# Kernel optimization log

Measured on AMD Instinct MI355X. Metric: run time of the kernel, lower is better.

The kernel has to match this reference:

```python
import jax, jax.numpy as jnp
import numpy as np
from jax import lax

B, ENC, H, E, V = 16, 64, 96, 128, 32000

def _same_pad(k):
    # PyTorch padding='same' (stride=1): low = (k-1)//2, high = (k-1) - low
    t = k - 1
    return (t // 2, t - t // 2)

def _conv(x, w, pad):
    return lax.conv_general_dilated(x, w, (1, 1), pad,
                                    dimension_numbers=('NCHW', 'OIHW', 'NCHW'))

def setup_inputs() -> dict:
    key = jax.random.key(0)
    ks = jax.random.split(key, 16)
    s = 0.05
    return {
        'encoder_outputs': jax.random.normal(ks[0], (B, ENC, H), jnp.float32),
        'input_ids': jax.random.randint(ks[1], (B,), 0, V),
        'hidden': jax.random.normal(ks[2], (1, B, H), jnp.float32),
        'coverage': jnp.zeros((B, ENC), jnp.float32),
        'emb': jax.random.normal(ks[3], (V, E), jnp.float32) * s,
        'W_dec': jax.random.normal(ks[4], (H, H), jnp.float32) * s,
        'b_dec': jnp.zeros((H,), jnp.float32),
        'attn_w': jax.random.normal(ks[5], (ENC, ENC, H, H), jnp.float32) * 0.003,
        'attn_b': jnp.zeros((ENC,), jnp.float32),
        'cvg_w': jax.random.normal(ks[6], (ENC, ENC, 1, H), jnp.float32) * s,
        'cvg_b': jnp.zeros((ENC,), jnp.float32),
        'v': jax.random.normal(ks[7], (B, H), jnp.float32) * s,
        'W_new': jax.random.normal(ks[8], (H, H + E), jnp.float32) * s,
        'b_new': jnp.zeros((H,), jnp.float32),
        'w_ih': jax.random.normal(ks[9], (3 * H, H), jnp.float32) * s,
        'w_hh': jax.random.normal(ks[10], (3 * H, H), jnp.float32) * s,
        'b_ih': jnp.zeros((3 * H,), jnp.float32),
        'b_hh': jnp.zeros((3 * H,), jnp.float32),
        'W_pre': jax.random.normal(ks[11], (H, 2 * H), jnp.float32) * s,
        'b_pre': jnp.zeros((H,), jnp.float32),
        'W_out': jax.random.normal(ks[12], (V, H), jnp.float32) * s,
        'b_out': jnp.zeros((V,), jnp.float32),
    }

def _attn(hidden, enc_out, coverage, W_dec, b_dec, attn_w, attn_b, cvg_w, cvg_b, v):
    # AttnCalc.forward
    ph, pw = _same_pad(H), _same_pad(H)
    enc_feat = _conv(enc_out.reshape(B, ENC, 1, H), attn_w, (ph, pw))
    enc_feat = enc_feat + attn_b[None, :, None, None]          # (B,ENC,1,H)
    dec_feat = (hidden[0] @ W_dec.T + b_dec).reshape(B, 1, 1, H)
    cvg_feat = _conv(coverage.reshape(B, ENC, 1, 1), cvg_w, ((0, 0), _same_pad(H)))
    cvg_feat = cvg_feat + cvg_b[None, :, None, None]           # (B,ENC,1,1)
    feats = jnp.tanh((enc_feat + dec_feat + cvg_feat).reshape(B, ENC, H))
    attn_weights = jax.nn.softmax(jnp.einsum('beh,bh->be', feats, v), axis=1)
    new_cov = coverage + attn_weights                          # in-place += in torch
    ctx = jnp.einsum('be,beh->bh', attn_weights, enc_out)      # (B,H)
    return ctx, attn_weights, new_cov

def reference(encoder_outputs, input_ids, hidden, coverage, emb, W_dec, b_dec,
              attn_w, attn_b, cvg_w, cvg_b, v, W_new, b_new,
              w_ih, w_hh, b_ih, b_hh, W_pre, b_pre, W_out, b_out):
    embedded = emb[input_ids]                                  # (B,E); dropout = identity (eval)
    ctx1, _, cov1 = _attn(hidden, encoder_outputs, coverage,
                          W_dec, b_dec, attn_w, attn_b, cvg_w, cvg_b, v)
    x = jnp.concatenate([embedded, ctx1], axis=1) @ W_new.T + b_new   # (B,H)
    # single GRU step (PyTorch gate order: r, z, n)
    h = hidden[0]
    gi = x @ w_ih.T + b_ih
    gh = h @ w_hh.T + b_hh
    r = jax.nn.sigmoid(gi[:, :H] + gh[:, :H])
    z = jax.nn.sigmoid(gi[:, H:2 * H] + gh[:, H:2 * H])
    n = jnp.tanh(gi[:, 2 * H:] + r * gh[:, 2 * H:])
    h_new = (1.0 - z) * n + z * h                              # (B,H)
    hidden_new = h_new[None]                                   # (1,B,H)
    ctx2, aw2, cov2 = _attn(hidden_new, encoder_outputs, cov1,
                            W_dec, b_dec, attn_w, attn_b, cvg_w, cvg_b, v)
    o = jnp.tanh(jnp.concatenate([h_new, ctx2], axis=1) @ W_pre.T + b_pre)
    logp = jax.nn.log_softmax(o @ W_out.T + b_out, axis=1)     # (B,V)
    return (logp, hidden_new, ctx2, aw2, cov2)
```

## Files before the change

### kernel.cpp

```cpp
#include <hip/hip_runtime.h>

#define BB 16
#define ENC 64
#define HH 96
#define EE 128
#define VV 32000

__global__ __launch_bounds__(256) void k_prep(
    const float* __restrict__ cvg_w, float* __restrict__ enc_feat,
    float* __restrict__ cvgw47)
{
    int idx = blockIdx.x * 256 + threadIdx.x;
    if (idx < BB * ENC * HH) enc_feat[idx] = 0.f;
    int e = idx - BB * ENC * HH;
    if (e >= 0 && e < ENC * ENC) cvgw47[e] = cvg_w[e * HH + 47];
}

__global__ __launch_bounds__(128) void k_encfeat(
    const float* __restrict__ enc,
    const float* __restrict__ attn_w,
    float* __restrict__ enc_feat)
{
    int blk = blockIdx.x;
    int b   = blk >> 7;
    int rem = blk & 127;
    int o0  = (rem >> 3) * 4;
    int i0  = (rem & 7) * 8;

    __shared__ float encS[8 * 192];
    __shared__ __align__(16) float Wb[4 * 8 * 96];

    for (int f = threadIdx.x; f < 8 * 192; f += 128) encS[f] = 0.f;
    __syncthreads();
    for (int f = threadIdx.x; f < 8 * 96; f += 128) {
        int i = f / 96, j = f - i * 96;
        encS[i * 192 + 47 + j] = enc[(size_t)((b * ENC + i0 + i) * 96) + j];
    }
    for (int f4 = threadIdx.x; f4 < 768; f4 += 128) {
        int f = f4 * 4;
        int o = f / 768;
        int r = f - o * 768;
        int i = r / 96, k = r - i * 96;
        float4 q = *(const float4*)(attn_w +
            ((size_t)((o0 + o) * ENC + (i0 + i)) * 96 + 47) * 96 + k);
        *(float4*)&Wb[f] = q;
    }
    __syncthreads();

    int x = threadIdx.x;
    if (x < 96) {
        float a0 = 0.f, a1 = 0.f, a2 = 0.f, a3 = 0.f;
        for (int i = 0; i < 8; ++i) {
            const float* er = &encS[i * 192 + x];
            const float* w0 = &Wb[0 * 768 + i * 96];
            const float* w1 = &Wb[1 * 768 + i * 96];
            const float* w2 = &Wb[2 * 768 + i * 96];
            const float* w3 = &Wb[3 * 768 + i * 96];
            #pragma unroll 6
            for (int c = 0; c < 24; ++c) {
                float e0 = er[4 * c + 0], e1 = er[4 * c + 1];
                float e2 = er[4 * c + 2], e3 = er[4 * c + 3];
                float4 q0 = *(const float4*)&w0[4 * c];
                float4 q1 = *(const float4*)&w1[4 * c];
                float4 q2 = *(const float4*)&w2[4 * c];
                float4 q3 = *(const float4*)&w3[4 * c];
                a0 += e0 * q0.x + e1 * q0.y + e2 * q0.z + e3 * q0.w;
                a1 += e0 * q1.x + e1 * q1.y + e2 * q1.z + e3 * q1.w;
                a2 += e0 * q2.x + e1 * q2.y + e2 * q2.z + e3 * q2.w;
                a3 += e0 * q3.x + e1 * q3.y + e2 * q3.z + e3 * q3.w;
            }
        }
        float* outr = enc_feat + (size_t)(b * ENC + o0) * 96 + x;
        unsafeAtomicAdd(outr + 0 * 96, a0);
        unsafeAtomicAdd(outr + 1 * 96, a1);
        unsafeAtomicAdd(outr + 2 * 96, a2);
        unsafeAtomicAdd(outr + 3 * 96, a3);
    }
}

__device__ __forceinline__ void matvec4(int g, int q, int nout, int nk,
    const float* __restrict__ W, int ldw, const float* __restrict__ bias,
    const float* __restrict__ xv, float* __restrict__ y)
{
    for (int j = g; j < nout; j += 64) {
        const float* wr = W + (size_t)j * ldw;
        float s = 0.f;
        for (int m = q; m < nk / 4; m += 4) {
            float4 wq = *(const float4*)(wr + 4 * m);
            s += wq.x * xv[4 * m] + wq.y * xv[4 * m + 1]
               + wq.z * xv[4 * m + 2] + wq.w * xv[4 * m + 3];
        }
        s += __shfl_xor(s, 1);
        s += __shfl_xor(s, 2);
        if (q == 0) y[j] = s + bias[j];
    }
}

__global__ __launch_bounds__(256) void k_fused(
    const float* __restrict__ enc, const int* __restrict__ ids,
    const float* __restrict__ hidden, const float* __restrict__ coverage,
    const float* __restrict__ emb,
    const float* __restrict__ W_dec, const float* __restrict__ b_dec,
    const float* __restrict__ attn_b,
    const float* __restrict__ cvgw47, const float* __restrict__ cvg_b,
    const float* __restrict__ vvec,
    const float* __restrict__ W_new, const float* __restrict__ b_new,
    const float* __restrict__ w_ih, const float* __restrict__ w_hh,
    const float* __restrict__ b_ih, const float* __restrict__ b_hh,
    const float* __restrict__ W_pre, const float* __restrict__ b_pre,
    const float* __restrict__ enc_feat, float* __restrict__ oG,
    float* __restrict__ out_hidden, float* __restrict__ out_ctx2,
    float* __restrict__ out_aw2, float* __restrict__ out_cov2)
{
    int b = blockIdx.x, t = threadIdx.x;
    int g = t >> 2, q = t & 3;

    __shared__ __align__(16) float efS[ENC * HH];
    __shared__ __align__(16) float encS[ENC * HH];
    __shared__ float hS[HH], vS[HH], decS[HH], ctxS[HH], xS[HH], h2S[HH], ctx2S[HH];
    __shared__ float covS[ENC], cvgS[ENC], sS[ENC], awS[ENC];
    __shared__ float embS[EE];
    __shared__ __align__(16) float xcatS[EE + HH];
    __shared__ float giS[3 * HH], ghS[3 * HH];

    for (int f = t; f < ENC * HH; f += 256) {
        efS[f]  = enc_feat[(size_t)b * ENC * HH + f];
        encS[f] = enc[(size_t)b * ENC * HH + f];
    }
    if (t < HH) { hS[t] = hidden[b * HH + t]; vS[t] = vvec[b * HH + t]; }
    if (t >= 96 && t < 160) covS[t - 96] = coverage[b * ENC + (t - 96)];
    if (t >= 128 && t < 256) embS[t - 128] = emb[(size_t)ids[b] * EE + (t - 128)];
    __syncthreads();

    matvec4(g, q, HH, HH, W_dec, HH, b_dec, hS, decS);
    matvec4(g, q, ENC, ENC, cvgw47, ENC, cvg_b, covS, cvgS);
    __syncthreads();
    {
        int e = g;
        float base = attn_b[e] + cvgS[e];
        const float* efr = &efS[e * HH];
        float s = 0.f;
        for (int m = q; m < 24; m += 4) {
            #pragma unroll
            for (int u = 0; u < 4; ++u) {
                int xx = 4 * m + u;
                s += tanhf(efr[xx] + decS[xx] + base) * vS[xx];
            }
        }
        s += __shfl_xor(s, 1); s += __shfl_xor(s, 2);
        if (q == 0) sS[e] = s;
    }
    __syncthreads();
    if (t < ENC) {
        float m = -1e30f;
        for (int j = 0; j < ENC; ++j) m = fmaxf(m, sS[j]);
        float sum = 0.f;
        for (int j = 0; j < ENC; ++j) sum += expf(sS[j] - m);
        float aw = expf(sS[t] - m) / sum;
        awS[t] = aw;
        covS[t] += aw;
    }
    __syncthreads();
    if (t < HH) {
        float c = 0.f;
        for (int o = 0; o < ENC; ++o) c += awS[o] * encS[o * HH + t];
        ctxS[t] = c;
        xcatS[EE + t] = c;
    }
    if (t >= 128 && t < 256) xcatS[t - 128] = embS[t - 128];
    __syncthreads();

    matvec4(g, q, HH, EE + HH, W_new, EE + HH, b_new, xcatS, xS);
    __syncthreads();

    matvec4(g, q, 3 * HH, HH, w_ih, HH, b_ih, xS, giS);
    matvec4(g, q, 3 * HH, HH, w_hh, HH, b_hh, hS, ghS);
    __syncthreads();
    if (t < HH) {
        float r = 1.f / (1.f + expf(-(giS[t] + ghS[t])));
        float z = 1.f / (1.f + expf(-(giS[HH + t] + ghS[HH + t])));
        float n = tanhf(giS[2 * HH + t] + r * ghS[2 * HH + t]);
        float hn = (1.f - z) * n + z * hS[t];
        h2S[t] = hn;
        out_hidden[b * HH + t] = hn;
    }
    __syncthreads();

    matvec4(g, q, HH, HH, W_dec, HH, b_dec, h2S, decS);
    matvec4(g, q, ENC, ENC, cvgw47, ENC, cvg_b, covS, cvgS);
    __syncthreads();
    {
        int e = g;
        float base = attn_b[e] + cvgS[e];
        const float* efr = &efS[e * HH];
        float s = 0.f;
        for (int m = q; m < 24; m += 4) {
            #pragma unroll
            for (int u = 0; u < 4; ++u) {
                int xx = 4 * m + u;
                s += tanhf(efr[xx] + decS[xx] + base) * vS[xx];
            }
        }
        s += __shfl_xor(s, 1); s += __shfl_xor(s, 2);
        if (q == 0) sS[e] = s;
    }
    __syncthreads();
    if (t < ENC) {
        float m = -1e30f;
        for (int j = 0; j < ENC; ++j) m = fmaxf(m, sS[j]);
        float sum = 0.f;
        for (int j = 0; j < ENC; ++j) sum += expf(sS[j] - m);
        float aw = expf(sS[t] - m) / sum;
        awS[t] = aw;
        covS[t] += aw;
        out_aw2[b * ENC + t]  = aw;
        out_cov2[b * ENC + t] = covS[t];
    }
    __syncthreads();
    if (t < HH) {
        float c = 0.f;
        for (int o = 0; o < ENC; ++o) c += awS[o] * encS[o * HH + t];
        ctx2S[t] = c;
        out_ctx2[b * HH + t] = c;
        xcatS[t] = h2S[t];
        xcatS[HH + t] = c;
    }
    __syncthreads();

    for (int j = g; j < HH; j += 64) {
        const float* wr = W_pre + (size_t)j * (2 * HH);
        float s = 0.f;
        for (int m = q; m < (2 * HH) / 4; m += 4) {
            float4 wq = *(const float4*)(wr + 4 * m);
            s += wq.x * xcatS[4 * m] + wq.y * xcatS[4 * m + 1]
               + wq.z * xcatS[4 * m + 2] + wq.w * xcatS[4 * m + 3];
        }
        s += __shfl_xor(s, 1); s += __shfl_xor(s, 2);
        if (q == 0) oG[b * HH + j] = tanhf(s + b_pre[j]);
    }
}

__global__ __launch_bounds__(256) void k_logits(
    const float* __restrict__ oG, const float* __restrict__ W_out,
    const float* __restrict__ b_out, float* __restrict__ logits)
{
    __shared__ __align__(16) float oS[BB * HH];
    for (int i = threadIdx.x; i < BB * HH; i += 256) oS[i] = oG[i];
    __syncthreads();

    int v = blockIdx.x * 256 + threadIdx.x;
    const float4* row = (const float4*)(W_out + (size_t)v * HH);
    float acc[BB];
    #pragma unroll
    for (int b = 0; b < BB; ++b) acc[b] = 0.f;

    for (int c = 0; c < HH / 4; ++c) {
        float4 qv = row[c];
        #pragma unroll
        for (int b = 0; b < BB; ++b) {
            const float4 o0 = *(const float4*)&oS[b * HH + c * 4];
            acc[b] += qv.x * o0.x + qv.y * o0.y + qv.z * o0.z + qv.w * o0.w;
        }
    }
    float bo = b_out[v];
    #pragma unroll
    for (int b = 0; b < BB; ++b) logits[b * VV + v] = acc[b] + bo;
}

__global__ __launch_bounds__(1024) void k_logsoftmax(float* __restrict__ out)
{
    int b = blockIdx.x, t = threadIdx.x;
    float* row = out + (size_t)b * VV;
    __shared__ float red[1024];

    float m = -1e30f;
    for (int v = t; v < VV; v += 1024) m = fmaxf(m, row[v]);
    red[t] = m; __syncthreads();
    for (int s = 512; s > 0; s >>= 1) {
        if (t < s) red[t] = fmaxf(red[t], red[t + s]);
        __syncthreads();
    }
    m = red[0]; __syncthreads();

    float sum = 0.f;
    for (int v = t; v < VV; v += 1024) sum += expf(row[v] - m);
    red[t] = sum; __syncthreads();
    for (int s = 512; s > 0; s >>= 1) {
        if (t < s) red[t] += red[t + s];
        __syncthreads();
    }
    float logZ = m + logf(red[0]);

    for (int v = t; v < VV; v += 1024) row[v] = row[v] - logZ;
}

extern "C" void kernel_launch(void* const* d_in, const int* in_sizes, int n_in,
                              void* d_out, int out_size, void* d_ws, size_t ws_size,
                              hipStream_t stream) {
    const float* enc    = (const float*)d_in[0];
    const int*   ids    = (const int*)d_in[1];
    const float* hidden = (const float*)d_in[2];
    const float* cover  = (const float*)d_in[3];
    const float* emb    = (const float*)d_in[4];
    const float* W_dec  = (const float*)d_in[5];
    const float* b_dec  = (const float*)d_in[6];
    const float* attn_w = (const float*)d_in[7];
    const float* attn_b = (const float*)d_in[8];
    const float* cvg_w  = (const float*)d_in[9];
    const float* cvg_b  = (const float*)d_in[10];
    const float* vvec   = (const float*)d_in[11];
    const float* W_new  = (const float*)d_in[12];
    const float* b_new  = (const float*)d_in[13];
    const float* w_ih   = (const float*)d_in[14];
    const float* w_hh   = (const float*)d_in[15];
    const float* b_ih   = (const float*)d_in[16];
    const float* b_hh   = (const float*)d_in[17];
    const float* W_pre  = (const float*)d_in[18];
    const float* b_pre  = (const float*)d_in[19];
    const float* W_out  = (const float*)d_in[20];
    const float* b_out  = (const float*)d_in[21];

    float* wsf      = (float*)d_ws;
    float* oG       = wsf;
    float* cvgw47   = wsf + 1536;
    float* enc_feat = wsf + 5632;

    float* out        = (float*)d_out;
    float* out_logp   = out;
    float* out_hidden = out + 512000;
    float* out_ctx2   = out + 513536;
    float* out_aw2    = out + 515072;
    float* out_cov2   = out + 516096;

    k_prep<<<400, 256, 0, stream>>>(cvg_w, enc_feat, cvgw47);
    k_encfeat<<<2048, 128, 0, stream>>>(enc, attn_w, enc_feat);
    k_fused<<<16, 256, 0, stream>>>(enc, ids, hidden, cover, emb, W_dec, b_dec,
                                    attn_b, cvgw47, cvg_b, vvec, W_new, b_new,
                                    w_ih, w_hh, b_ih, b_hh, W_pre, b_pre,
                                    enc_feat, oG,
                                    out_hidden, out_ctx2, out_aw2, out_cov2);
    k_logits<<<125, 256, 0, stream>>>(oG, W_out, b_out, out_logp);
    k_logsoftmax<<<16, 1024, 0, stream>>>(out_logp);
}
```

Before: 371.3 us.

## Replace enc_feat atomics with partial buffers, fold prep kernel, use fast math

The enc_feat convolution now writes per-input-chunk partial sums to a workspace instead of zero-initialising and atomically accumulating, and k_fused sums the 8 partials itself. This removes the k_prep launch and the atomics, and folds the cvg_w gather into k_encfeat. Each block now computes 8 output channels instead of 4, for more reuse of the enc row. tanh, sigmoid and exp switch to __expf-based approximations, and the log-softmax reductions get 4-way independent accumulators. The partial buffers cost extra workspace and extra reads in the 16-block fused kernel, and the fast math slightly changes numerics.

```diff
diff --git a/kernel.cpp b/kernel.cpp
--- a/kernel.cpp
+++ b/kernel.cpp
@@ -6,75 +6,77 @@
 #define EE 128
 #define VV 32000
 
-__global__ __launch_bounds__(256) void k_prep(
-    const float* __restrict__ cvg_w, float* __restrict__ enc_feat,
-    float* __restrict__ cvgw47)
-{
-    int idx = blockIdx.x * 256 + threadIdx.x;
-    if (idx < BB * ENC * HH) enc_feat[idx] = 0.f;
-    int e = idx - BB * ENC * HH;
-    if (e >= 0 && e < ENC * ENC) cvgw47[e] = cvg_w[e * HH + 47];
+__device__ __forceinline__ float tanh_fast(float x) {
+    float e = __expf(2.f * x);
+    return 1.f - 2.f / (e + 1.f);
+}
+__device__ __forceinline__ float sigmoid_fast(float x) {
+    return 1.f / (1.f + __expf(-x));
 }
 
 __global__ __launch_bounds__(128) void k_encfeat(
     const float* __restrict__ enc,
     const float* __restrict__ attn_w,
-    float* __restrict__ enc_feat)
+    const float* __restrict__ cvg_w,
+    float* __restrict__ part,
+    float* __restrict__ cvgw47)
 {
     int blk = blockIdx.x;
-    int b   = blk >> 7;
-    int rem = blk & 127;
-    int o0  = (rem >> 3) * 4;
-    int i0  = (rem & 7) * 8;
+    int b   = blk >> 6;
+    int ot  = (blk >> 3) & 7;
+    int ic  = blk & 7;
+    int o0  = ot * 8;
+    int i0  = ic * 8;
+    int t   = threadIdx.x;
 
     __shared__ float encS[8 * 192];
-    __shared__ __align__(16) float Wb[4 * 8 * 96];
-
-    for (int f = threadIdx.x; f < 8 * 192; f += 128) encS[f] = 0.f;
-    __syncthreads();
-    for (int f = threadIdx.x; f < 8 * 96; f += 128) {
+    __shared__ __align__(16) float Wb[8 * 8 * 96];
+
+    for (int f = t; f < 8 * 192; f += 128) encS[f] = 0.f;
+    __syncthreads();
+    for (int f = t; f < 8 * 96; f += 128) {
         int i = f / 96, j = f - i * 96;
         encS[i * 192 + 47 + j] = enc[(size_t)((b * ENC + i0 + i) * 96) + j];
     }
-    for (int f4 = threadIdx.x; f4 < 768; f4 += 128) {
-        int f = f4 * 4;
-        int o = f / 768;
-        int r = f - o * 768;
-        int i = r / 96, k = r - i * 96;
+    for (int f4 = t; f4 < 1536; f4 += 128) {
+        int o = f4 / 192;
+        int r = f4 - o * 192;
+        int i = r / 24, kq = r - i * 24;
         float4 q = *(const float4*)(attn_w +
-            ((size_t)((o0 + o) * ENC + (i0 + i)) * 96 + 47) * 96 + k);
-        *(float4*)&Wb[f] = q;
-    }
-    __syncthreads();
-
-    int x = threadIdx.x;
+            (size_t)((o0 + o) * ENC + (i0 + i)) * (96 * 96) + 47 * 96 + 4 * kq);
+        *(float4*)&Wb[(o * 8 + i) * 96 + 4 * kq] = q;
+    }
+    if (b == 0 && ot == 0) {
+        #pragma unroll
+        for (int j = 0; j < 4; ++j) {
+            int e = ic * 512 + j * 128 + t;
+            cvgw47[e] = cvg_w[(size_t)e * 96 + 47];
+        }
+    }
+    __syncthreads();
+
+    int x = t;
     if (x < 96) {
-        float a0 = 0.f, a1 = 0.f, a2 = 0.f, a3 = 0.f;
+        float acc[8];
+        #pragma unroll
+        for (int o = 0; o < 8; ++o) acc[o] = 0.f;
         for (int i = 0; i < 8; ++i) {
             const float* er = &encS[i * 192 + x];
-            const float* w0 = &Wb[0 * 768 + i * 96];
-            const float* w1 = &Wb[1 * 768 + i * 96];
-            const float* w2 = &Wb[2 * 768 + i * 96];
-            const float* w3 = &Wb[3 * 768 + i * 96];
-            #pragma unroll 6
+            const float* wb = &Wb[i * 96];
+            #pragma unroll 4
             for (int c = 0; c < 24; ++c) {
                 float e0 = er[4 * c + 0], e1 = er[4 * c + 1];
                 float e2 = er[4 * c + 2], e3 = er[4 * c + 3];
-                float4 q0 = *(const float4*)&w0[4 * c];
-                float4 q1 = *(const float4*)&w1[4 * c];
-                float4 q2 = *(const float4*)&w2[4 * c];
-                float4 q3 = *(const float4*)&w3[4 * c];
-                a0 += e0 * q0.x + e1 * q0.y + e2 * q0.z + e3 * q0.w;
-                a1 += e0 * q1.x + e1 * q1.y + e2 * q1.z + e3 * q1.w;
-                a2 += e0 * q2.x + e1 * q2.y + e2 * q2.z + e3 * q2.w;
-                a3 += e0 * q3.x + e1 * q3.y + e2 * q3.z + e3 * q3.w;
+                #pragma unroll
+                for (int o = 0; o < 8; ++o) {
+                    float4 q = *(const float4*)&wb[o * (8 * 96) + 4 * c];
+                    acc[o] += e0 * q.x + e1 * q.y + e2 * q.z + e3 * q.w;
+                }
             }
         }
-        float* outr = enc_feat + (size_t)(b * ENC + o0) * 96 + x;
-        unsafeAtomicAdd(outr + 0 * 96, a0);
-        unsafeAtomicAdd(outr + 1 * 96, a1);
-        unsafeAtomicAdd(outr + 2 * 96, a2);
-        unsafeAtomicAdd(outr + 3 * 96, a3);
+        float* outr = part + ((size_t)(ic * 16 + b) * 64 + o0) * 96 + x;
+        #pragma unroll
+        for (int o = 0; o < 8; ++o) outr[o * 96] = acc[o];
     }
 }
 
@@ -108,7 +110,7 @@
     const float* __restrict__ w_ih, const float* __restrict__ w_hh,
     const float* __restrict__ b_ih, const float* __restrict__ b_hh,
     const float* __restrict__ W_pre, const float* __restrict__ b_pre,
-    const float* __restrict__ enc_feat, float* __restrict__ oG,
+    const float* __restrict__ part, float* __restrict__ oG,
     float* __restrict__ out_hidden, float* __restrict__ out_ctx2,
     float* __restrict__ out_aw2, float* __restrict__ out_cov2)
 {
@@ -124,7 +126,11 @@
     __shared__ float giS[3 * HH], ghS[3 * HH];
 
     for (int f = t; f < ENC * HH; f += 256) {
-        efS[f]  = enc_feat[(size_t)b * ENC * HH + f];
+        float s = 0.f;
+        #pragma unroll
+        for (int ic = 0; ic < 8; ++ic)
+            s += part[(size_t)(ic * 16 + b) * (ENC * HH) + f];
+        efS[f]  = s;
         encS[f] = enc[(size_t)b * ENC * HH + f];
     }
     if (t < HH) { hS[t] = hidden[b * HH + t]; vS[t] = vvec[b * HH + t]; }
@@ -144,7 +150,7 @@
             #pragma unroll
             for (int u = 0; u < 4; ++u) {
                 int xx = 4 * m + u;
-                s += tanhf(efr[xx] + decS[xx] + base) * vS[xx];
+                s += tanh_fast(efr[xx] + decS[xx] + base) * vS[xx];
             }
         }
         s += __shfl_xor(s, 1); s += __shfl_xor(s, 2);
@@ -155,8 +161,8 @@
         float m = -1e30f;
         for (int j = 0; j < ENC; ++j) m = fmaxf(m, sS[j]);
         float sum = 0.f;
-        for (int j = 0; j < ENC; ++j) sum += expf(sS[j] - m);
-        float aw = expf(sS[t] - m) / sum;
+        for (int j = 0; j < ENC; ++j) sum += __expf(sS[j] - m);
+        float aw = __expf(sS[t] - m) / sum;
         awS[t] = aw;
         covS[t] += aw;
     }
@@ -177,9 +183,9 @@
     matvec4(g, q, 3 * HH, HH, w_hh, HH, b_hh, hS, ghS);
     __syncthreads();
     if (t < HH) {
-        float r = 1.f / (1.f + expf(-(giS[t] + ghS[t])));
-        float z = 1.f / (1.f + expf(-(giS[HH + t] + ghS[HH + t])));
-        float n = tanhf(giS[2 * HH + t] + r * ghS[2 * HH + t]);
+        float r = sigmoid_fast(giS[t] + ghS[t]);
+        float z = sigmoid_fast(giS[HH + t] + ghS[HH + t]);
+        float n = tanh_fast(giS[2 * HH + t] + r * ghS[2 * HH + t]);
         float hn = (1.f - z) * n + z * hS[t];
         h2S[t] = hn;
         out_hidden[b * HH + t] = hn;
@@ -198,7 +204,7 @@
             #pragma unroll
             for (int u = 0; u < 4; ++u) {
                 int xx = 4 * m + u;
-                s += tanhf(efr[xx] + decS[xx] + base) * vS[xx];
+                s += tanh_fast(efr[xx] + decS[xx] + base) * vS[xx];
             }
         }
         s += __shfl_xor(s, 1); s += __shfl_xor(s, 2);
@@ -209,8 +215,8 @@
         float m = -1e30f;
         for (int j = 0; j < ENC; ++j) m = fmaxf(m, sS[j]);
         float sum = 0.f;
-        for (int j = 0; j < ENC; ++j) sum += expf(sS[j] - m);
-        float aw = expf(sS[t] - m) / sum;
+        for (int j = 0; j < ENC; ++j) sum += __expf(sS[j] - m);
+        float aw = __expf(sS[t] - m) / sum;
         awS[t] = aw;
         covS[t] += aw;
         out_aw2[b * ENC + t]  = aw;
@@ -236,7 +242,7 @@
                + wq.z * xcatS[4 * m + 2] + wq.w * xcatS[4 * m + 3];
         }
         s += __shfl_xor(s, 1); s += __shfl_xor(s, 2);
-        if (q == 0) oG[b * HH + j] = tanhf(s + b_pre[j]);
+        if (q == 0) oG[b * HH + j] = tanh_fast(s + b_pre[j]);
     }
 }
 
@@ -254,6 +260,7 @@
     #pragma unroll
     for (int b = 0; b < BB; ++b) acc[b] = 0.f;
 
+    #pragma unroll 6
     for (int c = 0; c < HH / 4; ++c) {
         float4 qv = row[c];
         #pragma unroll
@@ -273,25 +280,41 @@
     float* row = out + (size_t)b * VV;
     __shared__ float red[1024];
 
-    float m = -1e30f;
-    for (int v = t; v < VV; v += 1024) m = fmaxf(m, row[v]);
-    red[t] = m; __syncthreads();
+    float m0 = -1e30f, m1 = -1e30f, m2 = -1e30f, m3 = -1e30f;
+    int v = t;
+    for (; v + 3072 < VV; v += 4096) {
+        m0 = fmaxf(m0, row[v]);
+        m1 = fmaxf(m1, row[v + 1024]);
+        m2 = fmaxf(m2, row[v + 2048]);
+        m3 = fmaxf(m3, row[v + 3072]);
+    }
+    for (; v < VV; v += 1024) m0 = fmaxf(m0, row[v]);
+    red[t] = fmaxf(fmaxf(m0, m1), fmaxf(m2, m3));
+    __syncthreads();
     for (int s = 512; s > 0; s >>= 1) {
         if (t < s) red[t] = fmaxf(red[t], red[t + s]);
         __syncthreads();
     }
-    m = red[0]; __syncthreads();
-
-    float sum = 0.f;
-    for (int v = t; v < VV; v += 1024) sum += expf(row[v] - m);
-    red[t] = sum; __syncthreads();
+    float m = red[0]; __syncthreads();
+
+    float s0 = 0.f, s1 = 0.f, s2 = 0.f, s3 = 0.f;
+    v = t;
+    for (; v + 3072 < VV; v += 4096) {
+        s0 += __expf(row[v] - m);
+        s1 += __expf(row[v + 1024] - m);
+        s2 += __expf(row[v + 2048] - m);
+        s3 += __expf(row[v + 3072] - m);
+    }
+    for (; v < VV; v += 1024) s0 += __expf(row[v] - m);
+    red[t] = (s0 + s1) + (s2 + s3);
+    __syncthreads();
     for (int s = 512; s > 0; s >>= 1) {
         if (t < s) red[t] += red[t + s];
         __syncthreads();
     }
     float logZ = m + logf(red[0]);
 
-    for (int v = t; v < VV; v += 1024) row[v] = row[v] - logZ;
+    for (v = t; v < VV; v += 1024) row[v] = row[v] - logZ;
 }
 
 extern "C" void kernel_launch(void* const* d_in, const int* in_sizes, int n_in,
@@ -320,10 +343,10 @@
     const float* W_out  = (const float*)d_in[20];
     const float* b_out  = (const float*)d_in[21];
 
-    float* wsf      = (float*)d_ws;
-    float* oG       = wsf;
-    float* cvgw47   = wsf + 1536;
-    float* enc_feat = wsf + 5632;
+    float* wsf    = (float*)d_ws;
+    float* oG     = wsf;
+    float* cvgw47 = wsf + 1536;
+    float* part   = wsf + 5632;
 
     float* out        = (float*)d_out;
     float* out_logp   = out;
@@ -332,12 +355,11 @@
     float* out_aw2    = out + 515072;
     float* out_cov2   = out + 516096;
 
-    k_prep<<<400, 256, 0, stream>>>(cvg_w, enc_feat, cvgw47);
-    k_encfeat<<<2048, 128, 0, stream>>>(enc, attn_w, enc_feat);
+    k_encfeat<<<1024, 128, 0, stream>>>(enc, attn_w, cvg_w, part, cvgw47);
     k_fused<<<16, 256, 0, stream>>>(enc, ids, hidden, cover, emb, W_dec, b_dec,
                                     attn_b, cvgw47, cvg_b, vvec, W_new, b_new,
                                     w_ih, w_hh, b_ih, b_hh, W_pre, b_pre,
-                                    enc_feat, oG,
+                                    part, oG,
                                     out_hidden, out_ctx2, out_aw2, out_cov2);
     k_logits<<<125, 256, 0, stream>>>(oG, W_out, b_out, out_logp);
     k_logsoftmax<<<16, 1024, 0, stream>>>(out_logp);
```

Result: faster. 360.8 us (-2.8%).
